# Kernel tuning notes

Hardware: AMD Instinct MI355X
Metric: run time of the kernel (lower is better)

Reference implementation:

```python
import jax, jax.numpy as jnp
import numpy as np

GROUP = 64
DIM = 4096
N_HEADS = 32
N_KV = 8
HEAD_DIM = DIM // N_HEADS  # 128
N_REP = N_HEADS // N_KV    # 4
B = 1
S = 2048
THETA = 1e6


def _pack_q40(rng, out_f, in_f):
    """Random int4 weights packed Q4_0 style (two nibbles per int8) + per-group scales."""
    q = rng.integers(-7, 8, size=(out_f * in_f,)).reshape(-1, 2, GROUP)
    packed = ((q[:, 0] << 4) | (q[:, 1] & 15)).astype(np.int8)  # [out*in/group/2, group]
    scale = (np.abs(rng.standard_normal((out_f * in_f // GROUP, 1))) * 0.01 + 1e-3).astype(np.float32)
    return jnp.asarray(packed), jnp.asarray(scale)


def dequantize_q40(w, scale, shape):
    """Faithful port of torch dequantize_q40: arithmetic shifts sign-extend nibbles."""
    msb = jnp.right_shift(w, 4)                          # high nibble, sign-extended
    lsb = jnp.right_shift(jnp.left_shift(w, 4), 4)       # low nibble, sign-extended
    grp = jnp.concatenate([msb, lsb], axis=1).reshape(-1, GROUP)  # hstack then view(-1, group)
    return (grp.astype(scale.dtype) * scale).reshape(shape)


def setup_inputs() -> dict:
    rng = np.random.default_rng(0)
    wq, sq = _pack_q40(rng, N_HEADS * HEAD_DIM, DIM)
    wk, sk = _pack_q40(rng, N_KV * HEAD_DIM, DIM)
    wv, sv = _pack_q40(rng, N_KV * HEAD_DIM, DIM)
    wo, so = _pack_q40(rng, DIM, N_HEADS * HEAD_DIM)
    x = jnp.asarray(rng.standard_normal((B, S, DIM)), jnp.float32)
    inv_freq = 1.0 / (THETA ** (np.arange(0, HEAD_DIM, 2, dtype=np.float64) / HEAD_DIM))
    ang = np.outer(np.arange(S, dtype=np.float64), inv_freq)  # [S, HEAD_DIM/2]
    cos = jnp.asarray(np.cos(ang), jnp.float32)
    sin = jnp.asarray(np.sin(ang), jnp.float32)
    causal = np.triu(np.ones((S, S), dtype=bool), k=1)
    mask = jnp.asarray(np.where(causal, -1e9, 0.0), jnp.float32)
    return dict(x=x, wq=wq, sq=sq, wk=wk, sk=sk, wv=wv, sv=sv, wo=wo, so=so,
                cos=cos, sin=sin, mask=mask)


def _rotate_half(t):
    h = t.shape[-1] // 2
    return jnp.concatenate([-t[..., h:], t[..., :h]], axis=-1)


def reference(x, wq, sq, wk, sk, wv, sv, wo, so, cos, sin, mask):
    # Dequant-then-matmul QKV projections (weights stored as [out, in])
    Wq = dequantize_q40(wq, sq, (N_HEADS * HEAD_DIM, DIM))
    Wk = dequantize_q40(wk, sk, (N_KV * HEAD_DIM, DIM))
    Wv = dequantize_q40(wv, sv, (N_KV * HEAD_DIM, DIM))
    Wo = dequantize_q40(wo, so, (DIM, N_HEADS * HEAD_DIM))

    xq = (x @ Wq.T).reshape(B, S, N_HEADS, HEAD_DIM)
    xk = (x @ Wk.T).reshape(B, S, N_KV, HEAD_DIM)
    xv = (x @ Wv.T).reshape(B, S, N_KV, HEAD_DIM)

    # RoPE (rotate-half convention): cos/sin are [S, HEAD_DIM/2] -> cat to [S, HEAD_DIM]
    cosf = jnp.concatenate([cos, cos], axis=-1)[:, None, :]  # [S, 1, HEAD_DIM]
    sinf = jnp.concatenate([sin, sin], axis=-1)[:, None, :]
    xq = xq * cosf + _rotate_half(xq) * sinf
    xk = xk * cosf + _rotate_half(xk) * sinf

    # start_pos == 0 prefill: keys/values are the freshly projected xk/xv
    # GQA: repeat_interleave over the kv-head dim
    keys = jnp.repeat(xk, N_REP, axis=2)    # [B, S, N_HEADS, HEAD_DIM]
    values = jnp.repeat(xv, N_REP, axis=2)

    scores = jnp.einsum('bqhd,bkhd->bhqk', xq, keys) / np.float32(np.sqrt(HEAD_DIM))
    scores = scores + mask  # additive causal mask broadcast over [B, H]
    attn = jax.nn.softmax(scores, axis=-1)
    out = jnp.einsum('bhqk,bkhd->bqhd', attn, values).reshape(B, S, N_HEADS * HEAD_DIM)
    return out @ Wo.T
```

## Files before the change

kernel.cpp:

```cpp
#include <hip/hip_runtime.h>
#include <stdint.h>

#define DIMX 4096
#define NH   32
#define NKV  8
#define HD   128
#define SEQ  2048
#define QKVD 6144

typedef _Float16 h16;
typedef __attribute__((ext_vector_type(8))) _Float16 h16x8;
typedef __attribute__((ext_vector_type(4))) _Float16 h16x4;
typedef __attribute__((ext_vector_type(4))) float   f32x4;

__device__ __forceinline__ void gload_lds16(const void* g, void* l) {
  __builtin_amdgcn_global_load_lds(
      (const __attribute__((address_space(1))) void*)g,
      (__attribute__((address_space(3))) void*)l, 16, 0, 0);
}

template <int CTRL>
__device__ __forceinline__ float dpp_mv(float x) {
  int y = __builtin_amdgcn_mov_dpp(__builtin_bit_cast(int, x), CTRL, 0xF, 0xF, true);
  return __builtin_bit_cast(float, y);
}
__device__ __forceinline__ float red16_max(float x) {
  x = fmaxf(x, dpp_mv<0xB1>(x));
  x = fmaxf(x, dpp_mv<0x1B>(x));
  x = fmaxf(x, dpp_mv<0x141>(x));
  x = fmaxf(x, dpp_mv<0x140>(x));
  return x;
}
__device__ __forceinline__ float red16_sum(float x) {
  x += dpp_mv<0xB1>(x);
  x += dpp_mv<0x1B>(x);
  x += dpp_mv<0x141>(x);
  x += dpp_mv<0x140>(x);
  return x;
}

template <int PERM>
__device__ __forceinline__ void dq_unit(const void* __restrict__ w, const float* __restrict__ sc,
                                        h16* __restrict__ out, int u, int flag) {
  uint32_t b4;
  if (flag) {
    const int4 t = *(const int4*)((const int*)w + 4 * u);
    b4 = (uint32_t)(t.x & 0xFF) | ((uint32_t)(t.y & 0xFF) << 8) |
         ((uint32_t)(t.z & 0xFF) << 16) | ((uint32_t)(t.w & 0xFF) << 24);
  } else {
    b4 = ((const uint32_t*)w)[u];
  }
  int r = u >> 4;
  int p = (u & 15) * 4;
  float shi = sc[2 * r], slo = sc[2 * r + 1];
  h16x4 hi, lo;
#pragma unroll
  for (int j = 0; j < 4; ++j) {
    int by = (int)((b4 >> (8 * j)) & 0xFF);
    int hn = (by << 24) >> 28;
    int ln = (by << 28) >> 28;
    hi[j] = (h16)((float)hn * shi);
    lo[j] = (h16)((float)ln * slo);
  }
  size_t base;
  if (PERM) {
    int row  = r >> 5;
    int rowp = (row & ~127) | (((row & 63) << 1) | ((row >> 6) & 1));
    base = ((size_t)rowp << 12) + (size_t)((r & 31) << 7);
  } else {
    base = (size_t)r << 7;
  }
  *(h16x4*)(out + base + p)      = hi;
  *(h16x4*)(out + base + 64 + p) = lo;
}

#define U_WQ 2097152
#define U_WK 524288
#define U_WV 524288
#define U_WO 2097152

__global__ __launch_bounds__(256) void prep_all(
    const void* __restrict__ wq, const float* __restrict__ sq,
    const void* __restrict__ wk, const float* __restrict__ sk,
    const void* __restrict__ wv, const float* __restrict__ sv,
    const void* __restrict__ wo, const float* __restrict__ so,
    const float4* __restrict__ x,
    h16* __restrict__ Wqkv, h16* __restrict__ Wo, h16x4* __restrict__ xb) {
  __shared__ int sfl;
  if (threadIdx.x == 0) {
    int ok = 1;
    const int* wi = (const int*)wq;
    for (int i = 0; i < 64; ++i) {
      int v = wi[i];
      if (v < -128 || v > 127) ok = 0;
    }
    sfl = ok;
  }
  __syncthreads();
  const int fl = sfl;
  int u = blockIdx.x * 256 + threadIdx.x;
  if (u < U_WQ) { dq_unit<1>(wq, sq, Wqkv, u, fl); return; }
  u -= U_WQ;
  if (u < U_WK) { dq_unit<1>(wk, sk, Wqkv + 16777216, u, fl); return; }
  u -= U_WK;
  if (u < U_WV) { dq_unit<0>(wv, sv, Wqkv + 20971520, u, fl); return; }
  u -= U_WV;
  if (u < U_WO) { dq_unit<0>(wo, so, Wo, u, fl); return; }
  u -= U_WO;
  {
    float4 v = x[u];
    h16x4 o;
    o.x = (h16)v.x; o.y = (h16)v.y; o.z = (h16)v.z; o.w = (h16)v.w;
    xb[u] = o;
  }
}

template <typename OutT, int NT, int MODE>
__global__ __launch_bounds__(512, 2) void gemm_pipe(
    const h16* __restrict__ A, const h16* __restrict__ B, OutT* __restrict__ C,
    int N, int K,
    const float* __restrict__ cosb, const float* __restrict__ sinb,
    h16* __restrict__ vt) {
  constexpr int NSLOT = 4 + NT;
  constexpr int BUFH  = NSLOT * 4096;
  __shared__ __attribute__((aligned(16))) h16 SM[2 * BUFH];

  const int tid  = threadIdx.x;
  const int w    = tid >> 6, lane = tid & 63;
  const int wr   = w >> 1, wc = w & 1;
  const int quad = lane >> 4, l15 = lane & 15;
  const int axr  = l15 & 7;
  const int m0 = blockIdx.y * 256, n0 = blockIdx.x * (NT * 64);

  const h16* Ab = A + (size_t)m0 * K;
  const h16* Bb = B + (size_t)n0 * K;
  const int srow = tid >> 3;
  const int sg8  = ((tid & 7) ^ (srow & 7)) * 8;

  f32x4 acc[2][2][2][NT];
#pragma unroll
  for (int a = 0; a < 2; ++a)
#pragma unroll
    for (int b = 0; b < 2; ++b)
#pragma unroll
      for (int mt = 0; mt < 2; ++mt)
#pragma unroll
        for (int nt = 0; nt < NT; ++nt) acc[a][b][mt][nt] = (f32x4){0.f, 0.f, 0.f, 0.f};

  h16x8 af[2][2][2];
  h16x8 bf1[NT][2];
  h16x8 bf0E[NT][2], bf0O[NT][2];

#define STG(sl_, tile_) do {                                                        \
    const h16* g_ = ((sl_) < 4) ? (Ab + (size_t)((sl_) * 64) * K)                   \
                                : (Bb + (size_t)(((sl_) - 4) * 64) * K);            \
    char* d_ = (char*)(SM + ((tile_) & 1) * BUFH + (sl_) * 4096);                   \
    gload_lds16(g_ + (size_t)srow * K + (tile_) * 64 + sg8, d_ + tid * 16);         \
  } while (0)

#define LDA_(tile_, a_) do {                                                        \
    const h16* s_ = SM + ((tile_) & 1) * BUFH + wr * 4096;                          \
    _Pragma("unroll") for (int mt = 0; mt < 2; ++mt)                                \
    _Pragma("unroll") for (int ks = 0; ks < 2; ++ks)                                \
      af[a_][mt][ks] = *(const h16x8*)&s_[((a_) * 32 + mt * 16 + l15) * 64 +        \
                                          (((ks * 4 + quad) ^ axr) * 8)];           \
  } while (0)

#define LDB1_(tile_) do {                                                           \
    const h16* s_ = SM + ((tile_) & 1) * BUFH + 16384;                              \
    _Pragma("unroll") for (int nt = 0; nt < NT; ++nt)                               \
    _Pragma("unroll") for (int ks = 0; ks < 2; ++ks)                                \
      bf1[nt][ks] = *(const h16x8*)&s_[(NT * 32 + wc * (NT * 16) + nt * 16 + l15) * 64 + \
                                       (((ks * 4 + quad) ^ axr) * 8)];              \
  } while (0)

#define LDB0_(tile_, D_) do {                                                       \
    const h16* s_ = SM + ((tile_) & 1) * BUFH + 16384;                              \
    _Pragma("unroll") for (int nt = 0; nt < NT; ++nt)                               \
    _Pragma("unroll") for (int ks = 0; ks < 2; ++ks)                                \
      D_[nt][ks] = *(const h16x8*)&s_[(wc * (NT * 16) + nt * 16 + l15) * 64 +       \
                                      (((ks * 4 + quad) ^ axr) * 8)];               \
  } while (0)

#define MMAB1(a_) do {                                                              \
    __builtin_amdgcn_s_setprio(1);                                                  \
    _Pragma("unroll") for (int mt = 0; mt < 2; ++mt)                                \
    _Pragma("unroll") for (int nt = 0; nt < NT; ++nt)                               \
    _Pragma("unroll") for (int ks = 0; ks < 2; ++ks)                                \
      acc[a_][1][mt][nt] = __builtin_amdgcn_mfma_f32_16x16x32_f16(                  \
          af[a_][mt][ks], bf1[nt][ks], acc[a_][1][mt][nt], 0, 0, 0);                \
    __builtin_amdgcn_s_setprio(0);                                                  \
  } while (0)

#define MMAB0(a_, D_) do {                                                          \
    __builtin_amdgcn_s_setprio(1);                                                  \
    _Pragma("unroll") for (int mt = 0; mt < 2; ++mt)                                \
    _Pragma("unroll") for (int nt = 0; nt < NT; ++nt)                               \
    _Pragma("unroll") for (int ks = 0; ks < 2; ++ks)                                \
      acc[a_][0][mt][nt] = __builtin_amdgcn_mfma_f32_16x16x32_f16(                  \
          af[a_][mt][ks], D_[nt][ks], acc[a_][0][mt][nt], 0, 0, 0);                 \
    __builtin_amdgcn_s_setprio(0);                                                  \
  } while (0)

#define CFENCE asm volatile("" ::: "memory")
#define BARX do { CFENCE; __builtin_amdgcn_s_barrier(); CFENCE; } while (0)
#define W2 do { if constexpr (NT == 3) asm volatile("s_waitcnt vmcnt(7)" ::: "memory"); \
                else                   asm volatile("s_waitcnt vmcnt(6)" ::: "memory"); } while (0)
#define W3 do { if constexpr (NT == 3) asm volatile("s_waitcnt vmcnt(3)" ::: "memory"); \
                else                   asm volatile("s_waitcnt vmcnt(2)" ::: "memory"); } while (0)
#define VM0  asm volatile("s_waitcnt vmcnt(0)" ::: "memory")

  const int NTILE = K >> 6;
  const int NIT   = K >> 7;

  STG(4, 0); STG(5, 0);
  if constexpr (NT == 3) STG(6, 0);
  STG(0, 0); STG(1, 0); STG(2, 0); STG(3, 0);
  STG(4, 1); STG(5, 1);
  if constexpr (NT == 3) STG(6, 1);
  STG(0, 1); STG(1, 1); STG(2, 1); STG(3, 1);
  W2;
  BARX;
  LDA_(0, 0); LDB0_(0, bf0E);

  for (int i = 0; i < NIT; ++i) {
    const int t0 = 2 * i, t1 = 2 * i + 1;
    const int T2 = (t0 + 2 < NTILE) ? t0 + 2 : NTILE - 1;
    const int T3 = (t1 + 2 < NTILE) ? t1 + 2 : NTILE - 1;
    LDB1_(t0);
    MMAB0(0, bf0E); BARX;
    LDA_(t0, 1); STG(4, T2); W2;
    MMAB1(0); BARX;
    LDB0_(t1, bf0O); STG(5, T2);
    if constexpr (NT == 3) STG(6, T2);
    W3;
    MMAB1(1); BARX;
    LDA_(t1, 0); STG(0, T2); STG(1, T2); STG(2, T2); STG(3, T2);
    MMAB0(1, bf0E); BARX;
    LDB1_(t1);
    MMAB0(0, bf0O); BARX;
    LDA_(t1, 1); STG(4, T3); W2;
    MMAB1(0); BARX;
    LDB0_(T2, bf0E); STG(5, T3);
    if constexpr (NT == 3) STG(6, T3);
    W3;
    MMAB1(1); BARX;
    LDA_(T2, 0); STG(0, T3); STG(1, T3); STG(2, T3); STG(3, T3);
    MMAB0(1, bf0O); BARX;
  }
  VM0;

  if constexpr (MODE == 1) {
#pragma unroll
    for (int a = 0; a < 2; ++a)
#pragma unroll
      for (int b = 0; b < 2; ++b)
#pragma unroll
        for (int mt = 0; mt < 2; ++mt)
#pragma unroll
          for (int nt = 0; nt < NT; ++nt) {
            const int cb   = n0 + b * (NT * 32) + wc * (NT * 16) + nt * 16;
            const int row0 = m0 + wr * 64 + a * 32 + mt * 16 + quad * 4;
            if (cb >= 5120) {
              const int dcol = cb + l15 - 5120;
              h16x4 vvv;
#pragma unroll
              for (int r = 0; r < 4; ++r) vvv[r] = (h16)acc[a][b][mt][nt][r];
              *(h16x4*)(vt + (size_t)dcol * SEQ + row0) = vvv;
            } else {
              const int col = cb + l15;
              const int j   = (col & 127) >> 1;
              const float sgn = (col & 1) ? 1.f : -1.f;
#pragma unroll
              for (int r = 0; r < 4; ++r) {
                float own = acc[a][b][mt][nt][r];
                float par = dpp_mv<0xB1>(own);
                float cc  = cosb[(size_t)(row0 + r) * 64 + j];
                float ss  = sinb[(size_t)(row0 + r) * 64 + j];
                C[(size_t)(row0 + r) * N + col] = (OutT)(own * cc + sgn * par * ss);
              }
            }
          }
  } else {
#pragma unroll
    for (int a = 0; a < 2; ++a)
#pragma unroll
      for (int b = 0; b < 2; ++b)
#pragma unroll
        for (int mt = 0; mt < 2; ++mt)
#pragma unroll
          for (int nt = 0; nt < NT; ++nt)
#pragma unroll
            for (int r = 0; r < 4; ++r) {
              int row = m0 + wr * 64 + a * 32 + mt * 16 + quad * 4 + r;
              int col = n0 + b * (NT * 32) + wc * (NT * 16) + nt * 16 + l15;
              C[(size_t)row * N + col] = (OutT)acc[a][b][mt][nt][r];
            }
  }
#undef STG
#undef LDA_
#undef LDB1_
#undef LDB0_
#undef MMAB1
#undef MMAB0
#undef CFENCE
#undef BARX
#undef W2
#undef W3
#undef VM0
}

__global__ __launch_bounds__(256, 2) void flash_attn(
    const h16* __restrict__ qkv, const h16* __restrict__ vt, h16* __restrict__ o_out) {
  __shared__ __attribute__((aligned(16))) h16 Ks[64 * 128];
  __shared__ __attribute__((aligned(16))) h16 Vts[128 * 64];
  __shared__ __attribute__((aligned(16))) h16 Ps[4][32 * 72];

  const int tid  = threadIdx.x;
  const int w    = tid >> 6, lane = tid & 63;
  const int quad = lane >> 4, l15 = lane & 15;
  const int h    = blockIdx.x;
  const int y    = blockIdx.y;
  const int qt   = (y < 8) ? (15 - y) : (y - 8);
  const int kv   = h >> 2;
  const int rowq = qt * 128 + w * 32;
  const h16* vtg = vt + (size_t)kv * HD * SEQ;

  h16x8 qf[2][4];
#pragma unroll
  for (int mt = 0; mt < 2; ++mt) {
    const h16* qrow = qkv + (size_t)(rowq + mt * 16 + l15) * QKVD + h * 128;
#pragma unroll
    for (int ks = 0; ks < 4; ++ks)
      qf[mt][ks] = *(const h16x8*)(qrow + ks * 32 + quad * 8);
  }

  f32x4 o[2][8];
#pragma unroll
  for (int mt = 0; mt < 2; ++mt)
#pragma unroll
    for (int i = 0; i < 8; ++i) o[mt][i] = (f32x4){0.f, 0.f, 0.f, 0.f};
  float mrow[2][4], lrow[2][4];
#pragma unroll
  for (int mt = 0; mt < 2; ++mt)
#pragma unroll
    for (int r = 0; r < 4; ++r) { mrow[mt][r] = -3e30f; lrow[mt][r] = 0.f; }
  h16* Psw = Ps[w];

  const int nkt = 2 * qt + 2;
  for (int kt = 0; kt < nkt; ++kt) {
    const int k0 = kt * 64;
    __syncthreads();
#pragma unroll
    for (int i = 0; i < 4; ++i) {
      int c = i * 256 + tid;
      int key = c >> 4, d8s = c & 15;
      gload_lds16(qkv + (size_t)(k0 + key) * QKVD + 4096 + kv * 128 + (d8s ^ (key & 15)) * 8,
                  (char*)Ks + c * 16);
    }
#pragma unroll
    for (int i = 0; i < 4; ++i) {
      int c = i * 256 + tid;
      int d = c >> 3, p = c & 7;
      gload_lds16(vtg + (size_t)d * SEQ + k0 + (p ^ (d & 7)) * 8,
                  (char*)Vts + c * 16);
    }
    __syncthreads();

    if (k0 <= rowq + 31) {
      const float sscale = 0.08838834764831845f;
      float alpha[2][4];
      f32x4 s2[2][4];
#pragma unroll
      for (int nt = 0; nt < 4; ++nt) {
        int key = nt * 16 + l15;
        f32x4 a0 = (f32x4){0.f, 0.f, 0.f, 0.f};
        f32x4 a1 = (f32x4){0.f, 0.f, 0.f, 0.f};
#pragma unroll
        for (int ks = 0; ks < 4; ++ks) {
          int d8 = ks * 4 + quad;
          h16x8 kf = *(const h16x8*)&Ks[key * 128 + ((d8 ^ (key & 15)) * 8)];
          a0 = __builtin_amdgcn_mfma_f32_16x16x32_f16(qf[0][ks], kf, a0, 0, 0, 0);
          a1 = __builtin_amdgcn_mfma_f32_16x16x32_f16(qf[1][ks], kf, a1, 0, 0, 0);
        }
        s2[0][nt] = a0;
        s2[1][nt] = a1;
      }
#pragma unroll
      for (int mt = 0; mt < 2; ++mt) {
#pragma unroll
        for (int r = 0; r < 4; ++r) {
          int rowg = rowq + mt * 16 + quad * 4 + r;
          float pv[4];
          float tm = -3e30f;
#pragma unroll
          for (int nt = 0; nt < 4; ++nt) {
            float v = s2[mt][nt][r] * sscale;
            if (k0 + nt * 16 + l15 > rowg) v = -3e30f;
            pv[nt] = v;
            tm = fmaxf(tm, v);
          }
          tm = red16_max(tm);
          float mnew = fmaxf(mrow[mt][r], tm);
          float a = __expf(mrow[mt][r] - mnew);
          mrow[mt][r] = mnew;
          alpha[mt][r] = a;
          float ps = 0.f;
#pragma unroll
          for (int nt = 0; nt < 4; ++nt) {
            float e = __expf(pv[nt] - mnew);
            ps += e;
            Psw[(mt * 16 + quad * 4 + r) * 72 + nt * 16 + l15] = (h16)e;
          }
          ps = red16_sum(ps);
          lrow[mt][r] = lrow[mt][r] * a + ps;
        }
      }
#pragma unroll
      for (int mt = 0; mt < 2; ++mt)
#pragma unroll
        for (int on = 0; on < 8; ++on) {
          o[mt][on][0] *= alpha[mt][0]; o[mt][on][1] *= alpha[mt][1];
          o[mt][on][2] *= alpha[mt][2]; o[mt][on][3] *= alpha[mt][3];
        }
      asm volatile("s_waitcnt lgkmcnt(0)" ::: "memory");
#pragma unroll
      for (int ks = 0; ks < 2; ++ks) {
        h16x8 pf0 = *(const h16x8*)&Psw[(0  + l15) * 72 + ks * 32 + quad * 8];
        h16x8 pf1 = *(const h16x8*)&Psw[(16 + l15) * 72 + ks * 32 + quad * 8];
        int k8 = ks * 4 + quad;
#pragma unroll
        for (int on = 0; on < 8; ++on) {
          int d = on * 16 + l15;
          h16x8 vf = *(const h16x8*)&Vts[d * 64 + ((k8 ^ (d & 7)) * 8)];
          o[0][on] = __builtin_amdgcn_mfma_f32_16x16x32_f16(pf0, vf, o[0][on], 0, 0, 0);
          o[1][on] = __builtin_amdgcn_mfma_f32_16x16x32_f16(pf1, vf, o[1][on], 0, 0, 0);
        }
      }
    }
  }
#pragma unroll
  for (int mt = 0; mt < 2; ++mt) {
    float linv[4];
#pragma unroll
    for (int r = 0; r < 4; ++r) linv[r] = 1.0f / lrow[mt][r];
#pragma unroll
    for (int on = 0; on < 8; ++on)
#pragma unroll
      for (int r = 0; r < 4; ++r) {
        int row = rowq + mt * 16 + quad * 4 + r;
        int col = h * 128 + on * 16 + l15;
        o_out[(size_t)row * DIMX + col] = (h16)(o[mt][on][r] * linv[r]);
      }
  }
}

extern "C" void kernel_launch(void* const* d_in, const int* in_sizes, int n_in,
                              void* d_out, int out_size, void* d_ws, size_t ws_size,
                              hipStream_t stream) {
  const float* x    = (const float*)d_in[0];
  const void*  wq   = d_in[1];
  const float* sq   = (const float*)d_in[2];
  const void*  wk   = d_in[3];
  const float* sk   = (const float*)d_in[4];
  const void*  wv   = d_in[5];
  const float* sv   = (const float*)d_in[6];
  const void*  wo   = d_in[7];
  const float* so   = (const float*)d_in[8];
  const float* cosb = (const float*)d_in[9];
  const float* sinb = (const float*)d_in[10];
  float* out = (float*)d_out;

  char* ws = (char*)d_ws;
  h16* Wqkv = (h16*)ws;
  h16* Wo   = (h16*)(ws + 50331648);
  h16* xb   = (h16*)(ws + 83886080);
  h16* qkv  = (h16*)(ws + 100663296);
  h16* vt   = (h16*)d_out;

  prep_all<<<28672, 256, 0, stream>>>(wq, sq, wk, sk, wv, sv, wo, so,
                                      (const float4*)x, Wqkv, Wo, (h16x4*)xb);

  gemm_pipe<h16, 3, 1><<<dim3(32, 8), 512, 0, stream>>>(
      xb, Wqkv, qkv, QKVD, DIMX, cosb, sinb, vt);

  flash_attn<<<dim3(32, 16), 256, 0, stream>>>(qkv, vt, xb);

  gemm_pipe<float, 2, 0><<<dim3(32, 8), 512, 0, stream>>>(
      xb, Wo, out, DIMX, DIMX, cosb, sinb, vt);
}
```

Measured before the change: 426.1 us.

## Register-prefetch K/V tiles, fold softmax scale into Q, lazy rescale, skip masking

K and V tiles for the next step are now loaded into registers during the current step's compute and written to LDS at the top of each iteration, replacing direct global-to-LDS loads. The 1/sqrt(d) softmax scale is moved into the QKV projection epilogue for Q columns. Causal masking runs only on diagonal tiles, and the running-max rescale of the output accumulators is skipped unless some row's max grows by more than 8. The prefetch costs 8 extra vector registers per thread and can lower occupancy. The thresholded rescale lets unnormalised values reach about e^8, which fp16 P tolerates but which trades some headroom for fewer multiplies.

After: 415.1 us. -2.6%, faster.

```diff
diff --git a/kernel.cpp b/kernel.cpp
--- a/kernel.cpp
+++ b/kernel.cpp
@@ -268,6 +268,7 @@
               for (int r = 0; r < 4; ++r) vvv[r] = (h16)acc[a][b][mt][nt][r];
               *(h16x4*)(vt + (size_t)dcol * SEQ + row0) = vvv;
             } else {
+              const float qs = (cb < 4096) ? 0.08838834764831845f : 1.0f;
               const int col = cb + l15;
               const int j   = (col & 127) >> 1;
               const float sgn = (col & 1) ? 1.f : -1.f;
@@ -277,7 +278,7 @@
                 float par = dpp_mv<0xB1>(own);
                 float cc  = cosb[(size_t)(row0 + r) * 64 + j];
                 float ss  = sinb[(size_t)(row0 + r) * 64 + j];
-                C[(size_t)(row0 + r) * N + col] = (OutT)(own * cc + sgn * par * ss);
+                C[(size_t)(row0 + r) * N + col] = (OutT)((own * cc + sgn * par * ss) * qs);
               }
             }
           }
@@ -347,28 +348,33 @@
     for (int r = 0; r < 4; ++r) { mrow[mt][r] = -3e30f; lrow[mt][r] = 0.f; }
   h16* Psw = Ps[w];
 
+  h16x8 kreg[4], vreg[4];
+#define LOADT(k0_) do {                                                              \
+    _Pragma("unroll") for (int i = 0; i < 4; ++i) {                                  \
+      int c = i * 256 + tid; int key = c >> 4, d8s = c & 15;                         \
+      kreg[i] = *(const h16x8*)(qkv + (size_t)((k0_) + key) * QKVD + 4096 +          \
+                                kv * 128 + ((d8s ^ (key & 15)) * 8));                \
+    }                                                                                \
+    _Pragma("unroll") for (int i = 0; i < 4; ++i) {                                  \
+      int c = i * 256 + tid; int d = c >> 3, p = c & 7;                              \
+      vreg[i] = *(const h16x8*)(vtg + (size_t)d * SEQ + (k0_) + ((p ^ (d & 7)) * 8));\
+    }                                                                                \
+  } while (0)
+
   const int nkt = 2 * qt + 2;
+  LOADT(0);
   for (int kt = 0; kt < nkt; ++kt) {
     const int k0 = kt * 64;
     __syncthreads();
 #pragma unroll
-    for (int i = 0; i < 4; ++i) {
-      int c = i * 256 + tid;
-      int key = c >> 4, d8s = c & 15;
-      gload_lds16(qkv + (size_t)(k0 + key) * QKVD + 4096 + kv * 128 + (d8s ^ (key & 15)) * 8,
-                  (char*)Ks + c * 16);
-    }
-#pragma unroll
-    for (int i = 0; i < 4; ++i) {
-      int c = i * 256 + tid;
-      int d = c >> 3, p = c & 7;
-      gload_lds16(vtg + (size_t)d * SEQ + k0 + (p ^ (d & 7)) * 8,
-                  (char*)Vts + c * 16);
-    }
+    for (int i = 0; i < 4; ++i) *(h16x8*)((char*)Ks + (i * 256 + tid) * 16) = kreg[i];
+#pragma unroll
+    for (int i = 0; i < 4; ++i) *(h16x8*)((char*)Vts + (i * 256 + tid) * 16) = vreg[i];
     __syncthreads();
+    const int knx = (kt + 1 < nkt) ? (kt + 1) * 64 : k0;
+    LOADT(knx);
 
     if (k0 <= rowq + 31) {
-      const float sscale = 0.08838834764831845f;
       float alpha[2][4];
       f32x4 s2[2][4];
 #pragma unroll
@@ -386,43 +392,69 @@
         s2[0][nt] = a0;
         s2[1][nt] = a1;
       }
+      const bool needmask = (k0 + 63 > rowq);
+      float tm2[2][4];
+      float need = -3e30f;
 #pragma unroll
       for (int mt = 0; mt < 2; ++mt) {
 #pragma unroll
         for (int r = 0; r < 4; ++r) {
-          int rowg = rowq + mt * 16 + quad * 4 + r;
-          float pv[4];
           float tm = -3e30f;
-#pragma unroll
-          for (int nt = 0; nt < 4; ++nt) {
-            float v = s2[mt][nt][r] * sscale;
-            if (k0 + nt * 16 + l15 > rowg) v = -3e30f;
-            pv[nt] = v;
-            tm = fmaxf(tm, v);
+          if (needmask) {
+            int rowg = rowq + mt * 16 + quad * 4 + r;
+#pragma unroll
+            for (int nt = 0; nt < 4; ++nt) {
+              float v = s2[mt][nt][r];
+              if (k0 + nt * 16 + l15 > rowg) v = -3e30f;
+              s2[mt][nt][r] = v;
+              tm = fmaxf(tm, v);
+            }
+          } else {
+#pragma unroll
+            for (int nt = 0; nt < 4; ++nt) tm = fmaxf(tm, s2[mt][nt][r]);
           }
           tm = red16_max(tm);
-          float mnew = fmaxf(mrow[mt][r], tm);
-          float a = __expf(mrow[mt][r] - mnew);
-          mrow[mt][r] = mnew;
-          alpha[mt][r] = a;
+          tm2[mt][r] = tm;
+          need = fmaxf(need, tm - mrow[mt][r]);
+        }
+      }
+      if (__any(need > 8.0f)) {
+#pragma unroll
+        for (int mt = 0; mt < 2; ++mt)
+#pragma unroll
+          for (int r = 0; r < 4; ++r) {
+            float mnew = fmaxf(mrow[mt][r], tm2[mt][r]);
+            alpha[mt][r] = __expf(mrow[mt][r] - mnew);
+            mrow[mt][r] = mnew;
+          }
+#pragma unroll
+        for (int mt = 0; mt < 2; ++mt)
+#pragma unroll
+          for (int on = 0; on < 8; ++on) {
+            o[mt][on][0] *= alpha[mt][0]; o[mt][on][1] *= alpha[mt][1];
+            o[mt][on][2] *= alpha[mt][2]; o[mt][on][3] *= alpha[mt][3];
+          }
+#pragma unroll
+        for (int mt = 0; mt < 2; ++mt)
+#pragma unroll
+          for (int r = 0; r < 4; ++r) lrow[mt][r] *= alpha[mt][r];
+      }
+#pragma unroll
+      for (int mt = 0; mt < 2; ++mt) {
+#pragma unroll
+        for (int r = 0; r < 4; ++r) {
+          float m = mrow[mt][r];
           float ps = 0.f;
 #pragma unroll
           for (int nt = 0; nt < 4; ++nt) {
-            float e = __expf(pv[nt] - mnew);
+            float e = __expf(s2[mt][nt][r] - m);
             ps += e;
             Psw[(mt * 16 + quad * 4 + r) * 72 + nt * 16 + l15] = (h16)e;
           }
           ps = red16_sum(ps);
-          lrow[mt][r] = lrow[mt][r] * a + ps;
+          lrow[mt][r] += ps;
         }
       }
-#pragma unroll
-      for (int mt = 0; mt < 2; ++mt)
-#pragma unroll
-        for (int on = 0; on < 8; ++on) {
-          o[mt][on][0] *= alpha[mt][0]; o[mt][on][1] *= alpha[mt][1];
-          o[mt][on][2] *= alpha[mt][2]; o[mt][on][3] *= alpha[mt][3];
-        }
       asm volatile("s_waitcnt lgkmcnt(0)" ::: "memory");
 #pragma unroll
       for (int ks = 0; ks < 2; ++ks) {
@@ -439,6 +471,7 @@
       }
     }
   }
+#undef LOADT
 #pragma unroll
   for (int mt = 0; mt < 2; ++mt) {
     float linv[4];
```
